# Performance work log

Hardware: AMD Instinct MI355X
Metric: run time of the kernel (lower is better)

## Reference

```python
import jax, jax.numpy as jnp
import numpy as np

B, S, H, F, E, N, K = 2, 4096, 1024, 3584, 8, 2, 2


def setup_inputs() -> dict:
    key = jax.random.key(0)
    ks = jax.random.split(key, 6)
    scale_h = 1.0 / np.sqrt(H)
    scale_f = 1.0 / np.sqrt(F)
    return {
        "hidden_states": jax.random.normal(ks[0], (B, S, H), dtype=jnp.float32),
        "gate_w": jax.random.normal(ks[1], (E, H), dtype=jnp.float32) * scale_h,
        "gate2_w": jax.random.normal(ks[2], (N, H), dtype=jnp.float32) * scale_h,
        "w1": jax.random.normal(ks[3], (E, F, H), dtype=jnp.float32) * scale_h,
        "w2": jax.random.normal(ks[4], (E, H, F), dtype=jnp.float32) * scale_f,
        "w3": jax.random.normal(ks[5], (E, F, H), dtype=jnp.float32) * scale_h,
    }


def reference(hidden_states, gate_w, gate2_w, w1, w2, w3):
    b, s, h = hidden_states.shape
    x = hidden_states.reshape(-1, h)  # [T, H]

    # Router: real gate + null-expert gate, concatenated
    router_logits = jnp.concatenate([x @ gate_w.T, x @ gate2_w.T], axis=1)  # [T, E+N]
    rw = jax.nn.softmax(router_logits.astype(jnp.float32), axis=1)
    top_w, sel = jax.lax.top_k(rw, K)  # [T, K]

    # Null experts (idx >= E) get their raw weight; real experts are renormalized
    mask = sel < E
    sw = top_w * mask
    denom = sw.sum(axis=-1, keepdims=True)
    denom = jnp.where(denom == 0, 1.0, denom)
    weights = (sw / denom + top_w * (~mask)).astype(x.dtype)  # [T, K]

    # Per-(token, real-expert) combine weight; null experts drop out (one_hot -> 0)
    combine = jnp.einsum("tke,tk->et", jax.nn.one_hot(sel, E, dtype=x.dtype), weights)  # [E, T]

    def body(acc, p):
        w1e, w2e, w3e, cw = p
        hgate = jax.nn.silu(x @ w1e.T) * (x @ w3e.T)  # [T, F]
        return acc + cw[:, None] * (hgate @ w2e.T), None

    out, _ = jax.lax.scan(body, jnp.zeros_like(x), (w1, w2, w3, combine))
    return out.reshape(b, s, h), router_logits
```

## Files before the change

kernel.cpp:

```cpp
#include <hip/hip_runtime.h>
#include <hip/hip_bf16.h>

namespace {

constexpr int T_TOK = 8192;
constexpr int HDIM  = 1024;
constexpr int FDIM  = 3584;
constexpr int CAP_ROWS = 17408;
constexpr int MAXMT = CAP_ROWS / 128;

typedef __bf16 bf16x8 __attribute__((ext_vector_type(8)));
typedef float  f32x4  __attribute__((ext_vector_type(4)));

__device__ inline unsigned short f2bf(float f) {
  union { float f; unsigned u; } a; a.f = f;
  unsigned r = a.u + 0x7fffu + ((a.u >> 16) & 1u);
  return (unsigned short)(r >> 16);
}

typedef const __attribute__((address_space(1))) void* gptr_t;
typedef __attribute__((address_space(3))) void* lptr_t;
__device__ inline void gload_lds16(const void* g, void* l) {
  __builtin_amdgcn_global_load_lds((gptr_t)g, (lptr_t)l, 16, 0, 0);
}

__global__ __launch_bounds__(256) void k_router(
    const float* __restrict__ x, const float* __restrict__ gw,
    const float* __restrict__ gw2, float* __restrict__ logits_out,
    int* __restrict__ sel, float* __restrict__ wts)
{
  int t = blockIdx.x * 4 + (threadIdx.x >> 6);
  int lane = threadIdx.x & 63;
  if (t >= T_TOK) return;
  const float* xr = x + (size_t)t * HDIM;
  float acc[10];
#pragma unroll
  for (int e = 0; e < 10; ++e) acc[e] = 0.f;
#pragma unroll
  for (int it = 0; it < 4; ++it) {
    int base = it * 256 + lane * 4;
    float4 xv = *reinterpret_cast<const float4*>(xr + base);
#pragma unroll
    for (int e = 0; e < 8; ++e) {
      float4 g = *reinterpret_cast<const float4*>(gw + e * HDIM + base);
      acc[e] += xv.x * g.x + xv.y * g.y + xv.z * g.z + xv.w * g.w;
    }
#pragma unroll
    for (int e = 0; e < 2; ++e) {
      float4 g = *reinterpret_cast<const float4*>(gw2 + e * HDIM + base);
      acc[8 + e] += xv.x * g.x + xv.y * g.y + xv.z * g.z + xv.w * g.w;
    }
  }
#pragma unroll
  for (int e = 0; e < 10; ++e) {
#pragma unroll
    for (int off = 32; off > 0; off >>= 1)
      acc[e] += __shfl_xor(acc[e], off, 64);
  }
  if (lane == 0) {
    float* lo = logits_out + (size_t)t * 10;
#pragma unroll
    for (int e = 0; e < 10; ++e) lo[e] = acc[e];
    float mx = acc[0];
#pragma unroll
    for (int e = 1; e < 10; ++e) mx = fmaxf(mx, acc[e]);
    float p[10], s = 0.f;
#pragma unroll
    for (int e = 0; e < 10; ++e) { p[e] = __expf(acc[e] - mx); s += p[e]; }
    float inv = 1.f / s;
#pragma unroll
    for (int e = 0; e < 10; ++e) p[e] *= inv;
    int i0 = 0;
    for (int e = 1; e < 10; ++e) if (p[e] > p[i0]) i0 = e;
    int i1 = (i0 == 0) ? 1 : 0;
    for (int e = 0; e < 10; ++e) if (e != i0 && p[e] > p[i1]) i1 = e;
    float w0 = p[i0], w1 = p[i1];
    bool r0 = i0 < 8, r1 = i1 < 8;
    float den = (r0 ? w0 : 0.f) + (r1 ? w1 : 0.f);
    if (den == 0.f) den = 1.f;
    sel[t * 2]     = i0; wts[t * 2]     = r0 ? w0 / den : 0.f;
    sel[t * 2 + 1] = i1; wts[t * 2 + 1] = r1 ? w1 / den : 0.f;
  }
}

__global__ __launch_bounds__(256) void k_histseg(
    const int* __restrict__ sel, int* __restrict__ meta)
{
  __shared__ int part[256][8];
  __shared__ int s_tile0[9];
  int tid = threadIdx.x;
  int c[8];
#pragma unroll
  for (int e = 0; e < 8; ++e) c[e] = 0;
  for (int i = 0; i < 64; ++i) {
    int v = sel[i * 256 + tid];
#pragma unroll
    for (int e = 0; e < 8; ++e) c[e] += (v == e);
  }
#pragma unroll
  for (int e = 0; e < 8; ++e) part[tid][e] = c[e];
  __syncthreads();
  for (int s = 128; s >= 1; s >>= 1) {
    if (tid < s) {
#pragma unroll
      for (int e = 0; e < 8; ++e) part[tid][e] += part[tid + s][e];
    }
    __syncthreads();
  }
  if (tid == 0) {
    int off = 0;
    for (int e = 0; e < 8; ++e) {
      int cnt = part[0][e];
      meta[e] = cnt;
      meta[8 + e] = 0;
      meta[16 + e] = off;
      s_tile0[e] = off >> 7;
      off += (cnt + 127) & ~127;
    }
    meta[24] = off;
    meta[25] = off >> 7;
    s_tile0[8] = off >> 7;
  }
  __syncthreads();
  int nt = s_tile0[8];
  if (tid < nt) {
    int e = 0;
    while (s_tile0[e + 1] <= tid) ++e;
    meta[32 + tid] = e;
  }
}

__global__ __launch_bounds__(256) void k_zeropad(
    const int* __restrict__ meta, unsigned short* __restrict__ xg)
{
  int e = blockIdx.x >> 7, r = blockIdx.x & 127;
  int c = meta[e];
  int pad = (c + 127) & ~127;
  if (c + r >= pad) return;
  size_t row = (size_t)meta[16 + e] + c + r;
  reinterpret_cast<ushort4*>(xg + row * HDIM)[threadIdx.x] = ushort4{0, 0, 0, 0};
}

__global__ __launch_bounds__(256) void k_scatter(
    const float* __restrict__ x, const int* __restrict__ sel,
    int* __restrict__ meta, int* __restrict__ pair_row,
    unsigned short* __restrict__ xg)
{
  __shared__ int s_cnt[8];
  __shared__ int s_base[8];
  __shared__ int s_row[256];
  int tid = threadIdx.x;
  int pair0 = blockIdx.x * 256;
  if (tid < 8) s_cnt[tid] = 0;
  __syncthreads();
  int e = sel[pair0 + tid];
  int rank = -1;
  if (e < 8) rank = atomicAdd(&s_cnt[e], 1);
  __syncthreads();
  if (tid < 8) {
    int c = s_cnt[tid];
    s_base[tid] = c > 0 ? atomicAdd(&meta[8 + tid], c) : 0;
  }
  __syncthreads();
  int row = (e < 8) ? meta[16 + e] + s_base[e] + rank : -1;
  pair_row[pair0 + tid] = row;
  s_row[tid] = row;
  __syncthreads();
  int wid = tid >> 6, lane = tid & 63;
  for (int i = wid; i < 256; i += 4) {
    int r = s_row[i];
    if (r < 0) continue;
    const float* xr = x + (size_t)((pair0 + i) >> 1) * HDIM;
    unsigned short* dst = xg + (size_t)r * HDIM;
#pragma unroll
    for (int it = 0; it < 4; ++it) {
      int base = it * 256 + lane * 4;
      float4 v = *reinterpret_cast<const float4*>(xr + base);
      ushort4 o{f2bf(v.x), f2bf(v.y), f2bf(v.z), f2bf(v.w)};
      *reinterpret_cast<ushort4*>(dst + base) = o;
    }
  }
}

__global__ __launch_bounds__(256) void k_conv3(
    const float* __restrict__ s1, const float* __restrict__ s3,
    const float* __restrict__ s2,
    unsigned short* __restrict__ d1, unsigned short* __restrict__ d3,
    unsigned short* __restrict__ d2,
    long long total, long long rl13, long long ss13,
    long long rl2, long long ss2)
{
  long long i = ((long long)blockIdx.x * 256 + threadIdx.x) * 8;
  if (i >= total) return;
  const float* src; unsigned short* dst; long long rowlen, sstride;
  if (blockIdx.y == 0)      { src = s1; dst = d1; rowlen = rl13; sstride = ss13; }
  else if (blockIdx.y == 1) { src = s3; dst = d3; rowlen = rl13; sstride = ss13; }
  else                      { src = s2; dst = d2; rowlen = rl2;  sstride = ss2;  }
  const float* sp;
  if (rowlen == sstride) {
    sp = src + i;
  } else {
    long long r = i / rowlen, c = i - r * rowlen;
    sp = src + r * sstride + c;
  }
  float4 a = reinterpret_cast<const float4*>(sp)[0];
  float4 b = reinterpret_cast<const float4*>(sp)[1];
  ushort4* d = reinterpret_cast<ushort4*>(dst + i);
  d[0] = ushort4{f2bf(a.x), f2bf(a.y), f2bf(a.z), f2bf(a.w)};
  d[1] = ushort4{f2bf(b.x), f2bf(b.y), f2bf(b.z), f2bf(b.w)};
}

__global__ __launch_bounds__(256) void k_gemm1(
    const unsigned short* __restrict__ xg,
    const unsigned short* __restrict__ wc1,
    const unsigned short* __restrict__ wc3,
    unsigned short* __restrict__ hg,
    const int* __restrict__ meta, int Fc)
{
  __shared__ unsigned short As[128 * 64];
  __shared__ unsigned short B1s[64 * 64];
  __shared__ unsigned short B3s[64 * 64];

  int mt = blockIdx.y;
  if (mt >= meta[25]) return;
  int e = meta[32 + mt];
  int mrow0 = mt * 128;
  int fl0 = blockIdx.x * 64;

  int tid = threadIdx.x, wid = tid >> 6, lane = tid & 63;
  int lr = lane & 15, lg = lane >> 4;
  int wm = wid >> 1, wn = wid & 1;

  f32x4 acc1[4][2], acc3[4][2];
  const f32x4 zero = {0.f, 0.f, 0.f, 0.f};
#pragma unroll
  for (int m = 0; m < 4; ++m)
#pragma unroll
    for (int n = 0; n < 2; ++n) { acc1[m][n] = zero; acc3[m][n] = zero; }

  const unsigned short* w1p = wc1 + ((size_t)e * Fc + fl0) * HDIM;
  const unsigned short* w3p = wc3 + ((size_t)e * Fc + fl0) * HDIM;

  int srow = tid >> 3;
  int sc8  = tid & 7;

  for (int k0 = 0; k0 < HDIM; k0 += 64) {
#pragma unroll
    for (int i = 0; i < 4; ++i) {
      int row = i * 32 + srow;
      int c8 = sc8 ^ (row & 7);
      gload_lds16(xg + (size_t)(mrow0 + row) * HDIM + k0 + c8 * 8,
                  (char*)As + i * 4096 + wid * 1024);
    }
#pragma unroll
    for (int i = 0; i < 2; ++i) {
      int row = i * 32 + srow;
      int c8 = sc8 ^ (row & 7);
      gload_lds16(w1p + (size_t)row * HDIM + k0 + c8 * 8,
                  (char*)B1s + i * 4096 + wid * 1024);
      gload_lds16(w3p + (size_t)row * HDIM + k0 + c8 * 8,
                  (char*)B3s + i * 4096 + wid * 1024);
    }
    __syncthreads();

#pragma unroll
    for (int kk = 0; kk < 2; ++kk) {
      bf16x8 a[4], b1[2], b3[2];
#pragma unroll
      for (int m = 0; m < 4; ++m) {
        int r = wm * 64 + m * 16 + lr;
        int off = r * 128 + ((kk * 64 + lg * 16) ^ ((r & 7) << 4));
        a[m] = *reinterpret_cast<const bf16x8*>((const char*)As + off);
      }
#pragma unroll
      for (int n = 0; n < 2; ++n) {
        int r = wn * 32 + n * 16 + lr;
        int off = r * 128 + ((kk * 64 + lg * 16) ^ ((r & 7) << 4));
        b1[n] = *reinterpret_cast<const bf16x8*>((const char*)B1s + off);
        b3[n] = *reinterpret_cast<const bf16x8*>((const char*)B3s + off);
      }
#pragma unroll
      for (int m = 0; m < 4; ++m)
#pragma unroll
        for (int n = 0; n < 2; ++n) {
          acc1[m][n] = __builtin_amdgcn_mfma_f32_16x16x32_bf16(a[m], b1[n], acc1[m][n], 0, 0, 0);
          acc3[m][n] = __builtin_amdgcn_mfma_f32_16x16x32_bf16(a[m], b3[n], acc3[m][n], 0, 0, 0);
        }
    }
    __syncthreads();
  }

#pragma unroll
  for (int m = 0; m < 4; ++m)
#pragma unroll
    for (int n = 0; n < 2; ++n) {
      int gcol = fl0 + wn * 32 + n * 16 + lr;
#pragma unroll
      for (int j = 0; j < 4; ++j) {
        int grow = mrow0 + wm * 64 + m * 16 + lg * 4 + j;
        float s1 = acc1[m][n][j];
        float s3 = acc3[m][n][j];
        float h = s1 / (1.f + __expf(-s1)) * s3;
        hg[(size_t)grow * Fc + gcol] = f2bf(h);
      }
    }
}

__global__ __launch_bounds__(256) void k_gemm2(
    const unsigned short* __restrict__ hg,
    const unsigned short* __restrict__ wc2,
    float* __restrict__ yrows, const int* __restrict__ meta,
    int Fc, int first)
{
  __shared__ unsigned short As[128 * 64];
  __shared__ unsigned short Bs[128 * 64];

  int mt = blockIdx.y;
  if (mt >= meta[25]) return;
  int e = meta[32 + mt];
  int mrow0 = mt * 128;
  int hcol0 = blockIdx.x * 128;

  int tid = threadIdx.x, wid = tid >> 6, lane = tid & 63;
  int lr = lane & 15, lg = lane >> 4;
  int wm = wid >> 1, wn = wid & 1;

  f32x4 acc[4][4];
  const f32x4 zero = {0.f, 0.f, 0.f, 0.f};
#pragma unroll
  for (int m = 0; m < 4; ++m)
#pragma unroll
    for (int n = 0; n < 4; ++n) acc[m][n] = zero;

  const unsigned short* w2p = wc2 + ((size_t)e * HDIM + hcol0) * Fc;

  int srow = tid >> 3;
  int sc8  = tid & 7;

  for (int k0 = 0; k0 < Fc; k0 += 64) {
#pragma unroll
    for (int i = 0; i < 4; ++i) {
      int row = i * 32 + srow;
      int c8 = sc8 ^ (row & 7);
      gload_lds16(hg + (size_t)(mrow0 + row) * Fc + k0 + c8 * 8,
                  (char*)As + i * 4096 + wid * 1024);
      gload_lds16(w2p + (size_t)row * Fc + k0 + c8 * 8,
                  (char*)Bs + i * 4096 + wid * 1024);
    }
    __syncthreads();

#pragma unroll
    for (int kk = 0; kk < 2; ++kk) {
      bf16x8 a[4], b[4];
#pragma unroll
      for (int m = 0; m < 4; ++m) {
        int r = wm * 64 + m * 16 + lr;
        int off = r * 128 + ((kk * 64 + lg * 16) ^ ((r & 7) << 4));
        a[m] = *reinterpret_cast<const bf16x8*>((const char*)As + off);
      }
#pragma unroll
      for (int n = 0; n < 4; ++n) {
        int r = wn * 64 + n * 16 + lr;
        int off = r * 128 + ((kk * 64 + lg * 16) ^ ((r & 7) << 4));
        b[n] = *reinterpret_cast<const bf16x8*>((const char*)Bs + off);
      }
#pragma unroll
      for (int m = 0; m < 4; ++m)
#pragma unroll
        for (int n = 0; n < 4; ++n)
          acc[m][n] = __builtin_amdgcn_mfma_f32_16x16x32_bf16(a[m], b[n], acc[m][n], 0, 0, 0);
    }
    __syncthreads();
  }

#pragma unroll
  for (int m = 0; m < 4; ++m)
#pragma unroll
    for (int n = 0; n < 4; ++n) {
      int gcol = hcol0 + wn * 64 + n * 16 + lr;
#pragma unroll
      for (int j = 0; j < 4; ++j) {
        int grow = mrow0 + wm * 64 + m * 16 + lg * 4 + j;
        float* yp = yrows + (size_t)grow * HDIM + gcol;
        float v = acc[m][n][j];
        if (first) *yp = v; else *yp += v;
      }
    }
}

__global__ __launch_bounds__(256) void k_combine(
    const float* __restrict__ yrows, const int* __restrict__ pair_row,
    const float* __restrict__ wts, float* __restrict__ out)
{
  int t = blockIdx.x * 4 + (threadIdx.x >> 6);
  int lane = threadIdx.x & 63;
  if (t >= T_TOK) return;
  int r0 = pair_row[t * 2], r1 = pair_row[t * 2 + 1];
  float w0 = (r0 >= 0) ? wts[t * 2] : 0.f;
  float w1 = (r1 >= 0) ? wts[t * 2 + 1] : 0.f;
  const float* y0 = yrows + (size_t)(r0 >= 0 ? r0 : 0) * HDIM;
  const float* y1 = yrows + (size_t)(r1 >= 0 ? r1 : 0) * HDIM;
  float* op = out + (size_t)t * HDIM;
#pragma unroll
  for (int it = 0; it < 4; ++it) {
    int base = it * 256 + lane * 4;
    float4 a = *reinterpret_cast<const float4*>(y0 + base);
    float4 b = *reinterpret_cast<const float4*>(y1 + base);
    float4 r{w0 * a.x + w1 * b.x, w0 * a.y + w1 * b.y,
             w0 * a.z + w1 * b.z, w0 * a.w + w1 * b.w};
    *reinterpret_cast<float4*>(op + base) = r;
  }
}

}

extern "C" void kernel_launch(void* const* d_in, const int* in_sizes, int n_in,
                              void* d_out, int out_size, void* d_ws, size_t ws_size,
                              hipStream_t stream)
{
  const float* x   = (const float*)d_in[0];
  const float* gw  = (const float*)d_in[1];
  const float* gw2 = (const float*)d_in[2];
  const float* w1  = (const float*)d_in[3];
  const float* w2  = (const float*)d_in[4];
  const float* w3  = (const float*)d_in[5];
  float* out = (float*)d_out;
  float* logits_out = out + (size_t)T_TOK * HDIM;

  char* p = (char*)d_ws;
  int* meta = (int*)p;            p += 1024;
  int* sel = (int*)p;             p += T_TOK * 2 * sizeof(int);
  float* wts = (float*)p;         p += T_TOK * 2 * sizeof(float);
  int* pair_row = (int*)p;        p += T_TOK * 2 * sizeof(int);
  unsigned short* xg = (unsigned short*)p;  p += (size_t)CAP_ROWS * HDIM * 2;
  float* yrows = (float*)p;                 p += (size_t)CAP_ROWS * HDIM * 4;
  size_t fixed = (size_t)(p - (char*)d_ws);

  int nf = 28;
  const int opts[6] = {1, 2, 4, 7, 14, 28};
  for (int i = 0; i < 6; ++i) {
    size_t Fc_i = FDIM / opts[i];
    size_t need = fixed + 3 * 16384 * Fc_i + (size_t)CAP_ROWS * Fc_i * 2;
    if (need <= ws_size) { nf = opts[i]; break; }
  }
  int Fc = FDIM / nf;

  unsigned short* wc1 = (unsigned short*)p;  p += (size_t)16384 * Fc;
  unsigned short* wc3 = (unsigned short*)p;  p += (size_t)16384 * Fc;
  unsigned short* wc2 = (unsigned short*)p;  p += (size_t)16384 * Fc;
  unsigned short* hg  = (unsigned short*)p;

  k_router<<<T_TOK / 4, 256, 0, stream>>>(x, gw, gw2, logits_out, sel, wts);
  k_histseg<<<1, 256, 0, stream>>>(sel, meta);
  k_zeropad<<<1024, 256, 0, stream>>>(meta, xg);
  k_scatter<<<T_TOK * 2 / 256, 256, 0, stream>>>(x, sel, meta, pair_row, xg);

  long long total = 8LL * Fc * HDIM;
  int ncb = (int)(total / 8 / 256);
  for (int c = 0; c < nf; ++c) {
    long long c0 = (long long)c * Fc;
    k_conv3<<<dim3(ncb, 3), 256, 0, stream>>>(
        w1 + c0 * HDIM, w3 + c0 * HDIM, w2 + c0, wc1, wc3, wc2,
        total, (long long)Fc * HDIM, (long long)FDIM * HDIM,
        (long long)Fc, (long long)FDIM);

    k_gemm1<<<dim3(Fc / 64, MAXMT), 256, 0, stream>>>(xg, wc1, wc3, hg, meta, Fc);
    k_gemm2<<<dim3(HDIM / 128, MAXMT), 256, 0, stream>>>(hg, wc2, yrows, meta, Fc, c == 0 ? 1 : 0);
  }
  k_combine<<<T_TOK / 4, 256, 0, stream>>>(yrows, pair_row, wts, out);
}
```

Baseline: 561.2 us.

## Double-buffer LDS tiles in both expert GEMMs to overlap loads with MFMA

Both grouped GEMM kernels now use a 64KB LDS region split into two stages. The next K-tile is issued via global_load_lds while the current one is computed, with s_waitcnt vmcnt(8) and raw barriers replacing the full __syncthreads wait. Per-row global pointers are precomputed and incremented, which removes the per-iteration address math. The aim is to hide global memory latency behind the MFMA work, at the cost of doubling LDS use, which may reduce the number of resident blocks per CU.

```diff
diff --git a/kernel.cpp b/kernel.cpp
--- a/kernel.cpp
+++ b/kernel.cpp
@@ -11,6 +11,8 @@
 
 typedef __bf16 bf16x8 __attribute__((ext_vector_type(8)));
 typedef float  f32x4  __attribute__((ext_vector_type(4)));
+
+#define CFENCE() asm volatile("" ::: "memory")
 
 __device__ inline unsigned short f2bf(float f) {
   union { float f; unsigned u; } a; a.f = f;
@@ -217,9 +219,7 @@
     unsigned short* __restrict__ hg,
     const int* __restrict__ meta, int Fc)
 {
-  __shared__ unsigned short As[128 * 64];
-  __shared__ unsigned short B1s[64 * 64];
-  __shared__ unsigned short B3s[64 * 64];
+  __shared__ __attribute__((aligned(128))) char lds[65536];
 
   int mt = blockIdx.y;
   if (mt >= meta[25]) return;
@@ -242,27 +242,38 @@
   const unsigned short* w3p = wc3 + ((size_t)e * Fc + fl0) * HDIM;
 
   int srow = tid >> 3;
-  int sc8  = tid & 7;
-
-  for (int k0 = 0; k0 < HDIM; k0 += 64) {
+  int c8 = (tid & 7) ^ (srow & 7);
+
+  const unsigned short* pa[4];
+  const unsigned short* pb1[2];
+  const unsigned short* pb3[2];
+#pragma unroll
+  for (int i = 0; i < 4; ++i)
+    pa[i] = xg + (size_t)(mrow0 + i * 32 + srow) * HDIM + c8 * 8;
+#pragma unroll
+  for (int i = 0; i < 2; ++i) {
+    pb1[i] = w1p + (size_t)(i * 32 + srow) * HDIM + c8 * 8;
+    pb3[i] = w3p + (size_t)(i * 32 + srow) * HDIM + c8 * 8;
+  }
+
+  auto STAGE = [&](int buf) {
+    char* base = lds + buf * 32768;
 #pragma unroll
     for (int i = 0; i < 4; ++i) {
-      int row = i * 32 + srow;
-      int c8 = sc8 ^ (row & 7);
-      gload_lds16(xg + (size_t)(mrow0 + row) * HDIM + k0 + c8 * 8,
-                  (char*)As + i * 4096 + wid * 1024);
+      gload_lds16(pa[i], base + i * 4096 + wid * 1024);
+      pa[i] += 64;
     }
 #pragma unroll
     for (int i = 0; i < 2; ++i) {
-      int row = i * 32 + srow;
-      int c8 = sc8 ^ (row & 7);
-      gload_lds16(w1p + (size_t)row * HDIM + k0 + c8 * 8,
-                  (char*)B1s + i * 4096 + wid * 1024);
-      gload_lds16(w3p + (size_t)row * HDIM + k0 + c8 * 8,
-                  (char*)B3s + i * 4096 + wid * 1024);
-    }
-    __syncthreads();
-
+      gload_lds16(pb1[i], base + 16384 + i * 4096 + wid * 1024);
+      pb1[i] += 64;
+      gload_lds16(pb3[i], base + 24576 + i * 4096 + wid * 1024);
+      pb3[i] += 64;
+    }
+  };
+
+  auto COMPUTE = [&](int buf) {
+    const char* base = lds + buf * 32768;
 #pragma unroll
     for (int kk = 0; kk < 2; ++kk) {
       bf16x8 a[4], b1[2], b3[2];
@@ -270,14 +281,14 @@
       for (int m = 0; m < 4; ++m) {
         int r = wm * 64 + m * 16 + lr;
         int off = r * 128 + ((kk * 64 + lg * 16) ^ ((r & 7) << 4));
-        a[m] = *reinterpret_cast<const bf16x8*>((const char*)As + off);
+        a[m] = *reinterpret_cast<const bf16x8*>(base + off);
       }
 #pragma unroll
       for (int n = 0; n < 2; ++n) {
         int r = wn * 32 + n * 16 + lr;
         int off = r * 128 + ((kk * 64 + lg * 16) ^ ((r & 7) << 4));
-        b1[n] = *reinterpret_cast<const bf16x8*>((const char*)B1s + off);
-        b3[n] = *reinterpret_cast<const bf16x8*>((const char*)B3s + off);
+        b1[n] = *reinterpret_cast<const bf16x8*>(base + 16384 + off);
+        b3[n] = *reinterpret_cast<const bf16x8*>(base + 24576 + off);
       }
 #pragma unroll
       for (int m = 0; m < 4; ++m)
@@ -287,8 +298,26 @@
           acc3[m][n] = __builtin_amdgcn_mfma_f32_16x16x32_bf16(a[m], b3[n], acc3[m][n], 0, 0, 0);
         }
     }
-    __syncthreads();
-  }
+  };
+
+  constexpr int NT = HDIM / 64;
+  int cur = 0;
+  STAGE(0);
+#pragma unroll 1
+  for (int t = 0; t < NT - 1; ++t) {
+    STAGE(cur ^ 1);
+    asm volatile("s_waitcnt vmcnt(8)" ::: "memory");
+    __builtin_amdgcn_s_barrier();
+    CFENCE();
+    COMPUTE(cur);
+    CFENCE();
+    __builtin_amdgcn_s_barrier();
+    cur ^= 1;
+  }
+  asm volatile("s_waitcnt vmcnt(0)" ::: "memory");
+  __builtin_amdgcn_s_barrier();
+  CFENCE();
+  COMPUTE(cur);
 
 #pragma unroll
   for (int m = 0; m < 4; ++m)
@@ -312,8 +341,7 @@
     float* __restrict__ yrows, const int* __restrict__ meta,
     int Fc, int first)
 {
-  __shared__ unsigned short As[128 * 64];
-  __shared__ unsigned short Bs[128 * 64];
+  __shared__ __attribute__((aligned(128))) char lds[65536];
 
   int mt = blockIdx.y;
   if (mt >= meta[25]) return;
@@ -335,20 +363,29 @@
   const unsigned short* w2p = wc2 + ((size_t)e * HDIM + hcol0) * Fc;
 
   int srow = tid >> 3;
-  int sc8  = tid & 7;
-
-  for (int k0 = 0; k0 < Fc; k0 += 64) {
+  int c8 = (tid & 7) ^ (srow & 7);
+
+  const unsigned short* pa[4];
+  const unsigned short* pb[4];
+#pragma unroll
+  for (int i = 0; i < 4; ++i) {
+    pa[i] = hg + (size_t)(mrow0 + i * 32 + srow) * Fc + c8 * 8;
+    pb[i] = w2p + (size_t)(i * 32 + srow) * Fc + c8 * 8;
+  }
+
+  auto STAGE = [&](int buf) {
+    char* base = lds + buf * 32768;
 #pragma unroll
     for (int i = 0; i < 4; ++i) {
-      int row = i * 32 + srow;
-      int c8 = sc8 ^ (row & 7);
-      gload_lds16(hg + (size_t)(mrow0 + row) * Fc + k0 + c8 * 8,
-                  (char*)As + i * 4096 + wid * 1024);
-      gload_lds16(w2p + (size_t)row * Fc + k0 + c8 * 8,
-                  (char*)Bs + i * 4096 + wid * 1024);
-    }
-    __syncthreads();
-
+      gload_lds16(pa[i], base + i * 4096 + wid * 1024);
+      pa[i] += 64;
+      gload_lds16(pb[i], base + 16384 + i * 4096 + wid * 1024);
+      pb[i] += 64;
+    }
+  };
+
+  auto COMPUTE = [&](int buf) {
+    const char* base = lds + buf * 32768;
 #pragma unroll
     for (int kk = 0; kk < 2; ++kk) {
       bf16x8 a[4], b[4];
@@ -356,13 +393,13 @@
       for (int m = 0; m < 4; ++m) {
         int r = wm * 64 + m * 16 + lr;
         int off = r * 128 + ((kk * 64 + lg * 16) ^ ((r & 7) << 4));
-        a[m] = *reinterpret_cast<const bf16x8*>((const char*)As + off);
+        a[m] = *reinterpret_cast<const bf16x8*>(base + off);
       }
 #pragma unroll
       for (int n = 0; n < 4; ++n) {
         int r = wn * 64 + n * 16 + lr;
         int off = r * 128 + ((kk * 64 + lg * 16) ^ ((r & 7) << 4));
-        b[n] = *reinterpret_cast<const bf16x8*>((const char*)Bs + off);
+        b[n] = *reinterpret_cast<const bf16x8*>(base + 16384 + off);
       }
 #pragma unroll
       for (int m = 0; m < 4; ++m)
@@ -370,8 +407,26 @@
         for (int n = 0; n < 4; ++n)
           acc[m][n] = __builtin_amdgcn_mfma_f32_16x16x32_bf16(a[m], b[n], acc[m][n], 0, 0, 0);
     }
-    __syncthreads();
-  }
+  };
+
+  int NT = Fc / 64;
+  int cur = 0;
+  STAGE(0);
+#pragma unroll 1
+  for (int t = 0; t < NT - 1; ++t) {
+    STAGE(cur ^ 1);
+    asm volatile("s_waitcnt vmcnt(8)" ::: "memory");
+    __builtin_amdgcn_s_barrier();
+    CFENCE();
+    COMPUTE(cur);
+    CFENCE();
+    __builtin_amdgcn_s_barrier();
+    cur ^= 1;
+  }
+  asm volatile("s_waitcnt vmcnt(0)" ::: "memory");
+  __builtin_amdgcn_s_barrier();
+  CFENCE();
+  COMPUTE(cur);
 
 #pragma unroll
   for (int m = 0; m < 4; ++m)
```

New measurement: 529.2 us. 5.7% less time.

## Use 32x32 MFMA in gate GEMM and double-buffer LDS in down GEMM

Applied to the files above, without the earlier changes.

The gate/up GEMM moves from 16x16x32 to 32x32x16 bf16 MFMA tiles, which cuts the number of LDS fragment loads per MFMA, and its epilogue is remapped to the 32x32 output layout. The down-projection GEMM gets two LDS buffers and a software pipeline: the next K tile is issued with global_load_lds while the current one is computed, using a partial vmcnt wait plus raw barriers in place of __syncthreads. This is meant to hide global-load latency behind MFMA work. The cost is twice the LDS (64KB per block), which can lower occupancy, and hand-tuned waitcnt ordering that is fragile.

```diff
diff --git a/kernel.cpp b/kernel.cpp
--- a/kernel.cpp
+++ b/kernel.cpp
@@ -11,6 +11,9 @@
 
 typedef __bf16 bf16x8 __attribute__((ext_vector_type(8)));
 typedef float  f32x4  __attribute__((ext_vector_type(4)));
+typedef float  f32x16 __attribute__((ext_vector_type(16)));
+
+#define CFENCE() asm volatile("" ::: "memory")
 
 __device__ inline unsigned short f2bf(float f) {
   union { float f; unsigned u; } a; a.f = f;
@@ -23,6 +26,8 @@
 __device__ inline void gload_lds16(const void* g, void* l) {
   __builtin_amdgcn_global_load_lds((gptr_t)g, (lptr_t)l, 16, 0, 0);
 }
+
+#define MFMA32(a, b, c) __builtin_amdgcn_mfma_f32_32x32x16_bf16(a, b, c, 0, 0, 0)
 
 __global__ __launch_bounds__(256) void k_router(
     const float* __restrict__ x, const float* __restrict__ gw,
@@ -228,15 +233,14 @@
   int fl0 = blockIdx.x * 64;
 
   int tid = threadIdx.x, wid = tid >> 6, lane = tid & 63;
-  int lr = lane & 15, lg = lane >> 4;
+  int l31 = lane & 31, lh = lane >> 5;
   int wm = wid >> 1, wn = wid & 1;
 
-  f32x4 acc1[4][2], acc3[4][2];
-  const f32x4 zero = {0.f, 0.f, 0.f, 0.f};
-#pragma unroll
-  for (int m = 0; m < 4; ++m)
-#pragma unroll
-    for (int n = 0; n < 2; ++n) { acc1[m][n] = zero; acc3[m][n] = zero; }
+  f32x16 acc1[2], acc3[2];
+#pragma unroll
+  for (int m = 0; m < 2; ++m)
+#pragma unroll
+    for (int j = 0; j < 16; ++j) { acc1[m][j] = 0.f; acc3[m][j] = 0.f; }
 
   const unsigned short* w1p = wc1 + ((size_t)e * Fc + fl0) * HDIM;
   const unsigned short* w3p = wc3 + ((size_t)e * Fc + fl0) * HDIM;
@@ -264,46 +268,35 @@
     __syncthreads();
 
 #pragma unroll
-    for (int kk = 0; kk < 2; ++kk) {
-      bf16x8 a[4], b1[2], b3[2];
-#pragma unroll
-      for (int m = 0; m < 4; ++m) {
-        int r = wm * 64 + m * 16 + lr;
-        int off = r * 128 + ((kk * 64 + lg * 16) ^ ((r & 7) << 4));
-        a[m] = *reinterpret_cast<const bf16x8*>((const char*)As + off);
+    for (int ks = 0; ks < 4; ++ks) {
+      int rb = wn * 32 + l31;
+      int kb_b = (ks * 32 + lh * 16) ^ ((rb & 7) << 4);
+      bf16x8 b1 = *reinterpret_cast<const bf16x8*>((const char*)B1s + rb * 128 + kb_b);
+      bf16x8 b3 = *reinterpret_cast<const bf16x8*>((const char*)B3s + rb * 128 + kb_b);
+#pragma unroll
+      for (int m = 0; m < 2; ++m) {
+        int ra = wm * 64 + m * 32 + l31;
+        int kb_a = (ks * 32 + lh * 16) ^ ((ra & 7) << 4);
+        bf16x8 a = *reinterpret_cast<const bf16x8*>((const char*)As + ra * 128 + kb_a);
+        acc1[m] = MFMA32(a, b1, acc1[m]);
+        acc3[m] = MFMA32(a, b3, acc3[m]);
       }
-#pragma unroll
-      for (int n = 0; n < 2; ++n) {
-        int r = wn * 32 + n * 16 + lr;
-        int off = r * 128 + ((kk * 64 + lg * 16) ^ ((r & 7) << 4));
-        b1[n] = *reinterpret_cast<const bf16x8*>((const char*)B1s + off);
-        b3[n] = *reinterpret_cast<const bf16x8*>((const char*)B3s + off);
-      }
-#pragma unroll
-      for (int m = 0; m < 4; ++m)
-#pragma unroll
-        for (int n = 0; n < 2; ++n) {
-          acc1[m][n] = __builtin_amdgcn_mfma_f32_16x16x32_bf16(a[m], b1[n], acc1[m][n], 0, 0, 0);
-          acc3[m][n] = __builtin_amdgcn_mfma_f32_16x16x32_bf16(a[m], b3[n], acc3[m][n], 0, 0, 0);
-        }
     }
     __syncthreads();
   }
 
 #pragma unroll
-  for (int m = 0; m < 4; ++m)
-#pragma unroll
-    for (int n = 0; n < 2; ++n) {
-      int gcol = fl0 + wn * 32 + n * 16 + lr;
-#pragma unroll
-      for (int j = 0; j < 4; ++j) {
-        int grow = mrow0 + wm * 64 + m * 16 + lg * 4 + j;
-        float s1 = acc1[m][n][j];
-        float s3 = acc3[m][n][j];
-        float h = s1 / (1.f + __expf(-s1)) * s3;
-        hg[(size_t)grow * Fc + gcol] = f2bf(h);
-      }
-    }
+  for (int m = 0; m < 2; ++m) {
+    int gcol = fl0 + wn * 32 + l31;
+#pragma unroll
+    for (int r = 0; r < 16; ++r) {
+      int grow = mrow0 + wm * 64 + m * 32 + (r & 3) + 8 * (r >> 2) + 4 * lh;
+      float s1 = acc1[m][r];
+      float s3 = acc3[m][r];
+      float h = s1 / (1.f + __expf(-s1)) * s3;
+      hg[(size_t)grow * Fc + gcol] = f2bf(h);
+    }
+  }
 }
 
 __global__ __launch_bounds__(256) void k_gemm2(
@@ -312,8 +305,7 @@
     float* __restrict__ yrows, const int* __restrict__ meta,
     int Fc, int first)
 {
-  __shared__ unsigned short As[128 * 64];
-  __shared__ unsigned short Bs[128 * 64];
+  __shared__ __attribute__((aligned(128))) char lds[65536];
 
   int mt = blockIdx.y;
   if (mt >= meta[25]) return;
@@ -335,20 +327,29 @@
   const unsigned short* w2p = wc2 + ((size_t)e * HDIM + hcol0) * Fc;
 
   int srow = tid >> 3;
-  int sc8  = tid & 7;
-
-  for (int k0 = 0; k0 < Fc; k0 += 64) {
+  int c8 = (tid & 7) ^ (srow & 7);
+
+  const unsigned short* pa[4];
+  const unsigned short* pb[4];
+#pragma unroll
+  for (int i = 0; i < 4; ++i) {
+    pa[i] = hg + (size_t)(mrow0 + i * 32 + srow) * Fc + c8 * 8;
+    pb[i] = w2p + (size_t)(i * 32 + srow) * Fc + c8 * 8;
+  }
+
+  auto STAGE = [&](int buf) {
+    char* base = lds + buf * 32768;
 #pragma unroll
     for (int i = 0; i < 4; ++i) {
-      int row = i * 32 + srow;
-      int c8 = sc8 ^ (row & 7);
-      gload_lds16(hg + (size_t)(mrow0 + row) * Fc + k0 + c8 * 8,
-                  (char*)As + i * 4096 + wid * 1024);
-      gload_lds16(w2p + (size_t)row * Fc + k0 + c8 * 8,
-                  (char*)Bs + i * 4096 + wid * 1024);
-    }
-    __syncthreads();
-
+      gload_lds16(pa[i], base + i * 4096 + wid * 1024);
+      pa[i] += 64;
+      gload_lds16(pb[i], base + 16384 + i * 4096 + wid * 1024);
+      pb[i] += 64;
+    }
+  };
+
+  auto COMPUTE = [&](int buf) {
+    const char* base = lds + buf * 32768;
 #pragma unroll
     for (int kk = 0; kk < 2; ++kk) {
       bf16x8 a[4], b[4];
@@ -356,13 +357,13 @@
       for (int m = 0; m < 4; ++m) {
         int r = wm * 64 + m * 16 + lr;
         int off = r * 128 + ((kk * 64 + lg * 16) ^ ((r & 7) << 4));
-        a[m] = *reinterpret_cast<const bf16x8*>((const char*)As + off);
+        a[m] = *reinterpret_cast<const bf16x8*>(base + off);
       }
 #pragma unroll
       for (int n = 0; n < 4; ++n) {
         int r = wn * 64 + n * 16 + lr;
         int off = r * 128 + ((kk * 64 + lg * 16) ^ ((r & 7) << 4));
-        b[n] = *reinterpret_cast<const bf16x8*>((const char*)Bs + off);
+        b[n] = *reinterpret_cast<const bf16x8*>(base + 16384 + off);
       }
 #pragma unroll
       for (int m = 0; m < 4; ++m)
@@ -370,8 +371,26 @@
         for (int n = 0; n < 4; ++n)
           acc[m][n] = __builtin_amdgcn_mfma_f32_16x16x32_bf16(a[m], b[n], acc[m][n], 0, 0, 0);
     }
-    __syncthreads();
-  }
+  };
+
+  int NT = Fc / 64;
+  int cur = 0;
+  STAGE(0);
+#pragma unroll 1
+  for (int t = 0; t < NT - 1; ++t) {
+    STAGE(cur ^ 1);
+    asm volatile("s_waitcnt vmcnt(8)" ::: "memory");
+    __builtin_amdgcn_s_barrier();
+    CFENCE();
+    COMPUTE(cur);
+    CFENCE();
+    __builtin_amdgcn_s_barrier();
+    cur ^= 1;
+  }
+  asm volatile("s_waitcnt vmcnt(0)" ::: "memory");
+  __builtin_amdgcn_s_barrier();
+  CFENCE();
+  COMPUTE(cur);
 
 #pragma unroll
   for (int m = 0; m < 4; ++m)
```

Result: faster. 527.5 us (-6.0%).

## Fuse weighted combine into gemm2 via atomic scatter and double-buffer gemm2 loads

Applied to the files above, without the earlier changes.

Removes the intermediate fp32 yrows buffer and the combine kernel. gemm2 now scales each row by its routing weight and atomically adds it into the zero-initialised output at the owning token, using new per-row token and weight tables. Padded rows get zero weight and are skipped. gemm2's K loop also gains a double-buffered LDS pipeline with explicit vmcnt waits so loads overlap compute. The cost is float atomics to global memory (two experts per token contend) with nondeterministic summation order, plus an extra zeroing pass over the output.

```diff
diff --git a/kernel.cpp b/kernel.cpp
--- a/kernel.cpp
+++ b/kernel.cpp
@@ -11,6 +11,8 @@
 
 typedef __bf16 bf16x8 __attribute__((ext_vector_type(8)));
 typedef float  f32x4  __attribute__((ext_vector_type(4)));
+
+#define CFENCE() asm volatile("" ::: "memory")
 
 __device__ inline unsigned short f2bf(float f) {
   union { float f; unsigned u; } a; a.f = f;
@@ -84,10 +86,13 @@
 }
 
 __global__ __launch_bounds__(256) void k_histseg(
-    const int* __restrict__ sel, int* __restrict__ meta)
+    const int* __restrict__ sel, int* __restrict__ meta,
+    int* __restrict__ rowtok, float* __restrict__ roww)
 {
   __shared__ int part[256][8];
   __shared__ int s_tile0[9];
+  __shared__ int s_off[8];
+  __shared__ int s_c[8];
   int tid = threadIdx.x;
   int c[8];
 #pragma unroll
@@ -114,6 +119,8 @@
       meta[e] = cnt;
       meta[8 + e] = 0;
       meta[16 + e] = off;
+      s_off[e] = off;
+      s_c[e] = cnt;
       s_tile0[e] = off >> 7;
       off += (cnt + 127) & ~127;
     }
@@ -128,22 +135,25 @@
     while (s_tile0[e + 1] <= tid) ++e;
     meta[32 + tid] = e;
   }
-}
-
-__global__ __launch_bounds__(256) void k_zeropad(
-    const int* __restrict__ meta, unsigned short* __restrict__ xg)
-{
-  int e = blockIdx.x >> 7, r = blockIdx.x & 127;
-  int c = meta[e];
-  int pad = (c + 127) & ~127;
-  if (c + r >= pad) return;
-  size_t row = (size_t)meta[16 + e] + c + r;
-  reinterpret_cast<ushort4*>(xg + row * HDIM)[threadIdx.x] = ushort4{0, 0, 0, 0};
+  for (int idx = tid; idx < 8 * 128; idx += 256) {
+    int e = idx >> 7, j = idx & 127;
+    int cnt = s_c[e];
+    int pad = (cnt + 127) & ~127;
+    int pos = cnt + j;
+    if (pos < pad) { rowtok[s_off[e] + pos] = 0; roww[s_off[e] + pos] = 0.f; }
+  }
+}
+
+__global__ __launch_bounds__(256) void k_zero_out(float* __restrict__ out)
+{
+  size_t i = ((size_t)blockIdx.x * 256 + threadIdx.x) * 4;
+  *reinterpret_cast<float4*>(out + i) = float4{0.f, 0.f, 0.f, 0.f};
 }
 
 __global__ __launch_bounds__(256) void k_scatter(
     const float* __restrict__ x, const int* __restrict__ sel,
-    int* __restrict__ meta, int* __restrict__ pair_row,
+    const float* __restrict__ wts, int* __restrict__ meta,
+    int* __restrict__ rowtok, float* __restrict__ roww,
     unsigned short* __restrict__ xg)
 {
   __shared__ int s_cnt[8];
@@ -163,8 +173,11 @@
   }
   __syncthreads();
   int row = (e < 8) ? meta[16 + e] + s_base[e] + rank : -1;
-  pair_row[pair0 + tid] = row;
   s_row[tid] = row;
+  if (row >= 0) {
+    rowtok[row] = (pair0 + tid) >> 1;
+    roww[row] = wts[pair0 + tid];
+  }
   __syncthreads();
   int wid = tid >> 6, lane = tid & 63;
   for (int i = wid; i < 256; i += 4) {
@@ -180,6 +193,17 @@
       *reinterpret_cast<ushort4*>(dst + base) = o;
     }
   }
+}
+
+__global__ __launch_bounds__(256) void k_zeropad(
+    const int* __restrict__ meta, unsigned short* __restrict__ xg)
+{
+  int e = blockIdx.x >> 7, r = blockIdx.x & 127;
+  int c = meta[e];
+  int pad = (c + 127) & ~127;
+  if (c + r >= pad) return;
+  size_t row = (size_t)meta[16 + e] + c + r;
+  reinterpret_cast<ushort4*>(xg + row * HDIM)[threadIdx.x] = ushort4{0, 0, 0, 0};
 }
 
 __global__ __launch_bounds__(256) void k_conv3(
@@ -309,11 +333,11 @@
 __global__ __launch_bounds__(256) void k_gemm2(
     const unsigned short* __restrict__ hg,
     const unsigned short* __restrict__ wc2,
-    float* __restrict__ yrows, const int* __restrict__ meta,
-    int Fc, int first)
-{
-  __shared__ unsigned short As[128 * 64];
-  __shared__ unsigned short Bs[128 * 64];
+    float* __restrict__ out, const int* __restrict__ meta,
+    const int* __restrict__ rowtok, const float* __restrict__ roww,
+    int Fc)
+{
+  __shared__ __attribute__((aligned(128))) char lds[65536];
 
   int mt = blockIdx.y;
   if (mt >= meta[25]) return;
@@ -335,20 +359,29 @@
   const unsigned short* w2p = wc2 + ((size_t)e * HDIM + hcol0) * Fc;
 
   int srow = tid >> 3;
-  int sc8  = tid & 7;
-
-  for (int k0 = 0; k0 < Fc; k0 += 64) {
+  int c8 = (tid & 7) ^ (srow & 7);
+
+  const unsigned short* pa[4];
+  const unsigned short* pb[4];
+#pragma unroll
+  for (int i = 0; i < 4; ++i) {
+    pa[i] = hg + (size_t)(mrow0 + i * 32 + srow) * Fc + c8 * 8;
+    pb[i] = w2p + (size_t)(i * 32 + srow) * Fc + c8 * 8;
+  }
+
+  auto STAGE = [&](int buf) {
+    char* base = lds + buf * 32768;
 #pragma unroll
     for (int i = 0; i < 4; ++i) {
-      int row = i * 32 + srow;
-      int c8 = sc8 ^ (row & 7);
-      gload_lds16(hg + (size_t)(mrow0 + row) * Fc + k0 + c8 * 8,
-                  (char*)As + i * 4096 + wid * 1024);
-      gload_lds16(w2p + (size_t)row * Fc + k0 + c8 * 8,
-                  (char*)Bs + i * 4096 + wid * 1024);
-    }
-    __syncthreads();
-
+      gload_lds16(pa[i], base + i * 4096 + wid * 1024);
+      pa[i] += 64;
+      gload_lds16(pb[i], base + 16384 + i * 4096 + wid * 1024);
+      pb[i] += 64;
+    }
+  };
+
+  auto COMPUTE = [&](int buf) {
+    const char* base = lds + buf * 32768;
 #pragma unroll
     for (int kk = 0; kk < 2; ++kk) {
       bf16x8 a[4], b[4];
@@ -356,13 +389,13 @@
       for (int m = 0; m < 4; ++m) {
         int r = wm * 64 + m * 16 + lr;
         int off = r * 128 + ((kk * 64 + lg * 16) ^ ((r & 7) << 4));
-        a[m] = *reinterpret_cast<const bf16x8*>((const char*)As + off);
+        a[m] = *reinterpret_cast<const bf16x8*>(base + off);
       }
 #pragma unroll
       for (int n = 0; n < 4; ++n) {
         int r = wn * 64 + n * 16 + lr;
         int off = r * 128 + ((kk * 64 + lg * 16) ^ ((r & 7) << 4));
-        b[n] = *reinterpret_cast<const bf16x8*>((const char*)Bs + off);
+        b[n] = *reinterpret_cast<const bf16x8*>(base + 16384 + off);
       }
 #pragma unroll
       for (int m = 0; m < 4; ++m)
@@ -370,46 +403,42 @@
         for (int n = 0; n < 4; ++n)
           acc[m][n] = __builtin_amdgcn_mfma_f32_16x16x32_bf16(a[m], b[n], acc[m][n], 0, 0, 0);
     }
-    __syncthreads();
-  }
+  };
+
+  int NT = Fc / 64;
+  int cur = 0;
+  STAGE(0);
+#pragma unroll 1
+  for (int t = 0; t < NT - 1; ++t) {
+    STAGE(cur ^ 1);
+    asm volatile("s_waitcnt vmcnt(8)" ::: "memory");
+    __builtin_amdgcn_s_barrier();
+    CFENCE();
+    COMPUTE(cur);
+    CFENCE();
+    __builtin_amdgcn_s_barrier();
+    cur ^= 1;
+  }
+  asm volatile("s_waitcnt vmcnt(0)" ::: "memory");
+  __builtin_amdgcn_s_barrier();
+  CFENCE();
+  COMPUTE(cur);
 
 #pragma unroll
   for (int m = 0; m < 4; ++m)
 #pragma unroll
-    for (int n = 0; n < 4; ++n) {
-      int gcol = hcol0 + wn * 64 + n * 16 + lr;
-#pragma unroll
-      for (int j = 0; j < 4; ++j) {
-        int grow = mrow0 + wm * 64 + m * 16 + lg * 4 + j;
-        float* yp = yrows + (size_t)grow * HDIM + gcol;
-        float v = acc[m][n][j];
-        if (first) *yp = v; else *yp += v;
+    for (int j = 0; j < 4; ++j) {
+      int grow = mrow0 + wm * 64 + m * 16 + lg * 4 + j;
+      float w = roww[grow];
+      if (w != 0.f) {
+        float* ob = out + (size_t)rowtok[grow] * HDIM;
+#pragma unroll
+        for (int n = 0; n < 4; ++n) {
+          int gcol = hcol0 + wn * 64 + n * 16 + lr;
+          atomicAdd(ob + gcol, w * acc[m][n][j]);
+        }
       }
     }
-}
-
-__global__ __launch_bounds__(256) void k_combine(
-    const float* __restrict__ yrows, const int* __restrict__ pair_row,
-    const float* __restrict__ wts, float* __restrict__ out)
-{
-  int t = blockIdx.x * 4 + (threadIdx.x >> 6);
-  int lane = threadIdx.x & 63;
-  if (t >= T_TOK) return;
-  int r0 = pair_row[t * 2], r1 = pair_row[t * 2 + 1];
-  float w0 = (r0 >= 0) ? wts[t * 2] : 0.f;
-  float w1 = (r1 >= 0) ? wts[t * 2 + 1] : 0.f;
-  const float* y0 = yrows + (size_t)(r0 >= 0 ? r0 : 0) * HDIM;
-  const float* y1 = yrows + (size_t)(r1 >= 0 ? r1 : 0) * HDIM;
-  float* op = out + (size_t)t * HDIM;
-#pragma unroll
-  for (int it = 0; it < 4; ++it) {
-    int base = it * 256 + lane * 4;
-    float4 a = *reinterpret_cast<const float4*>(y0 + base);
-    float4 b = *reinterpret_cast<const float4*>(y1 + base);
-    float4 r{w0 * a.x + w1 * b.x, w0 * a.y + w1 * b.y,
-             w0 * a.z + w1 * b.z, w0 * a.w + w1 * b.w};
-    *reinterpret_cast<float4*>(op + base) = r;
-  }
 }
 
 }
@@ -431,9 +460,9 @@
   int* meta = (int*)p;            p += 1024;
   int* sel = (int*)p;             p += T_TOK * 2 * sizeof(int);
   float* wts = (float*)p;         p += T_TOK * 2 * sizeof(float);
-  int* pair_row = (int*)p;        p += T_TOK * 2 * sizeof(int);
+  int* rowtok = (int*)p;          p += CAP_ROWS * sizeof(int);
+  float* roww = (float*)p;        p += CAP_ROWS * sizeof(float);
   unsigned short* xg = (unsigned short*)p;  p += (size_t)CAP_ROWS * HDIM * 2;
-  float* yrows = (float*)p;                 p += (size_t)CAP_ROWS * HDIM * 4;
   size_t fixed = (size_t)(p - (char*)d_ws);
 
   int nf = 28;
@@ -451,9 +480,10 @@
   unsigned short* hg  = (unsigned short*)p;
 
   k_router<<<T_TOK / 4, 256, 0, stream>>>(x, gw, gw2, logits_out, sel, wts);
-  k_histseg<<<1, 256, 0, stream>>>(sel, meta);
+  k_histseg<<<1, 256, 0, stream>>>(sel, meta, rowtok, roww);
+  k_zero_out<<<T_TOK * HDIM / 4 / 256, 256, 0, stream>>>(out);
+  k_scatter<<<T_TOK * 2 / 256, 256, 0, stream>>>(x, sel, wts, meta, rowtok, roww, xg);
   k_zeropad<<<1024, 256, 0, stream>>>(meta, xg);
-  k_scatter<<<T_TOK * 2 / 256, 256, 0, stream>>>(x, sel, meta, pair_row, xg);
 
   long long total = 8LL * Fc * HDIM;
   int ncb = (int)(total / 8 / 256);
@@ -465,7 +495,6 @@
         (long long)Fc, (long long)FDIM);
 
     k_gemm1<<<dim3(Fc / 64, MAXMT), 256, 0, stream>>>(xg, wc1, wc3, hg, meta, Fc);
-    k_gemm2<<<dim3(HDIM / 128, MAXMT), 256, 0, stream>>>(hg, wc2, yrows, meta, Fc, c == 0 ? 1 : 0);
-  }
-  k_combine<<<T_TOK / 4, 256, 0, stream>>>(yrows, pair_row, wts, out);
-}
+    k_gemm2<<<dim3(HDIM / 128, MAXMT), 256, 0, stream>>>(hg, wc2, out, meta, rowtok, roww, Fc);
+  }
+}
```

New measurement: 538.3 us. 1.04x faster.
